# Kernel optimization log

Measured on AMD Instinct MI355X. Metric: run time of the kernel, lower is better.

## Reference

```python
import jax, jax.numpy as jnp
import numpy as np

DILATIONS = (1, 2, 4, 8, 16, 32, 64, 128)  # new_dilation doubles across all blocks*layers
BN_EPS = 1e-5


def conv1x1(x, w, b):
    # x: [B,C,N,T], w: [O,C], b: [O]
    return jnp.einsum('oc,bcnt->bont', w, x) + b[None, :, None, None]


def dilated_conv(x, w, b, d):
    T = x.shape[-1]
    y = jnp.einsum('oc,bcnt->bont', w[:, :, 0], x[..., :T - d]) \
      + jnp.einsum('oc,bcnt->bont', w[:, :, 1], x[..., d:])
    return y + b[None, :, None, None]


def graph_conv(x, supports, w, b):
    # gcn module, order=2, diag_mode='self_and_neighbor' (A unchanged), use_power=False
    outs = [x]
    for A in supports:
        h = x
        for _ in range(2):  # order
            h = jnp.einsum('bcvt,vw->bcwt', h, A)  # nconv: 'ncvl,vw->ncwl'
            outs.append(h)
    return conv1x1(jnp.concatenate(outs, axis=1), w, b)


def setup_inputs() -> dict:
    key = jax.random.key(0)
    B, Cin, N, T = 8, 2, 500, 256
    rc, dc, sc, ec, od, L, R = 32, 32, 256, 512, 12, 8, 10
    ks = jax.random.split(key, 24)
    s = 0.1
    return {
        'x': jax.random.normal(ks[0], (B, Cin, N, T), jnp.float32),
        'A0': jax.random.uniform(ks[1], (N, N), jnp.float32),
        'start_w': jax.random.normal(ks[2], (rc, Cin), jnp.float32) * s,
        'start_b': jnp.zeros((rc,), jnp.float32),
        'filt_w': jax.random.normal(ks[3], (L, dc, rc, 2), jnp.float32) * s,
        'filt_b': jnp.zeros((L, dc), jnp.float32),
        'gate_w': jax.random.normal(ks[4], (L, dc, rc, 2), jnp.float32) * s,
        'gate_b': jnp.zeros((L, dc), jnp.float32),
        'skip_w': jax.random.normal(ks[5], (L, sc, dc), jnp.float32) * s,
        'skip_b': jnp.zeros((L, sc), jnp.float32),
        'gcn_w': jax.random.normal(ks[6], (L, rc, 5 * dc), jnp.float32) * s,  # (order*supports+1)*c_in = 160
        'gcn_b': jnp.zeros((L, rc), jnp.float32),
        'bn_g': jnp.ones((L, rc), jnp.float32),
        'bn_b': jnp.zeros((L, rc), jnp.float32),
        'nodevec1': jax.random.normal(ks[7], (N, R), jnp.float32),
        'nodevec2': jax.random.normal(ks[8], (R, N), jnp.float32),
        'end1_w': jax.random.normal(ks[9], (ec, sc), jnp.float32) * s,
        'end1_b': jnp.zeros((ec,), jnp.float32),
        'end2_w': jax.random.normal(ks[10], (od, ec), jnp.float32) * s,
        'end2_b': jnp.zeros((od,), jnp.float32),
    }


def reference(x, A0, start_w, start_b, filt_w, filt_b, gate_w, gate_b,
              skip_w, skip_b, gcn_w, gcn_b, bn_g, bn_b,
              nodevec1, nodevec2, end1_w, end1_b, end2_w, end2_b):
    # adaptive adjacency: softmax(relu(E1 @ E2), dim=1)
    adp = jax.nn.softmax(jax.nn.relu(nodevec1 @ nodevec2), axis=1)
    supports = [A0, adp]

    h = conv1x1(x, start_w, start_b)  # [B,32,N,T]
    skip = None
    for i, d in enumerate(DILATIONS):
        residual = h
        f = jnp.tanh(dilated_conv(residual, filt_w[i], filt_b[i], d))
        g = jax.nn.sigmoid(dilated_conv(residual, gate_w[i], gate_b[i], d))
        h = f * g
        s = conv1x1(h, skip_w[i], skip_b[i])
        skip = s if skip is None else s + skip[..., -s.shape[-1]:]
        h = graph_conv(h, supports, gcn_w[i], gcn_b[i])
        h = h + residual[..., -h.shape[-1]:]
        # BatchNorm2d in eval mode: running_mean=0, running_var=1
        h = h / jnp.sqrt(1.0 + BN_EPS) * bn_g[i][None, :, None, None] + bn_b[i][None, :, None, None]

    out = jax.nn.relu(skip)
    out = jax.nn.relu(conv1x1(out, end1_w, end1_b))
    out = conv1x1(out, end2_w, end2_b)  # [B,12,N,1]
    return out
```

## Files before the change

kernel.cpp:

```cpp
#include <hip/hip_runtime.h>
#include <cstdint>
#include <cstddef>

#define NN 500
#define KP 512

typedef _Float16 f16;
typedef _Float16 half8 __attribute__((ext_vector_type(8)));
typedef float floatx4 __attribute__((ext_vector_type(4)));

struct PassSet {
  const f16* A[10];
  const f16* B[10];
};

__global__ __launch_bounds__(256) void adp_kernel(const float* __restrict__ e1,
                                                  const float* __restrict__ e2,
                                                  float* __restrict__ adp) {
  int r = blockIdx.x;
  int tid = threadIdx.x;
  __shared__ float red[256];
  __shared__ float e1row[16];
  if (tid < 10) e1row[tid] = e1[r * 10 + tid];
  __syncthreads();
  float z0, z1 = 0.f;
  {
    float acc = 0.f;
#pragma unroll
    for (int k = 0; k < 10; k++) acc += e1row[k] * e2[k * NN + tid];
    z0 = fmaxf(acc, 0.f);
  }
  bool has1 = (tid + 256) < NN;
  if (has1) {
    float acc = 0.f;
#pragma unroll
    for (int k = 0; k < 10; k++) acc += e1row[k] * e2[k * NN + tid + 256];
    z1 = fmaxf(acc, 0.f);
  }
  float mx = has1 ? fmaxf(z0, z1) : z0;
  red[tid] = mx;
  __syncthreads();
  for (int s = 128; s > 0; s >>= 1) {
    if (tid < s) red[tid] = fmaxf(red[tid], red[tid + s]);
    __syncthreads();
  }
  mx = red[0];
  __syncthreads();
  float ex0 = __expf(z0 - mx);
  float ex1 = has1 ? __expf(z1 - mx) : 0.f;
  red[tid] = ex0 + ex1;
  __syncthreads();
  for (int s = 128; s > 0; s >>= 1) {
    if (tid < s) red[tid] += red[tid + s];
    __syncthreads();
  }
  float inv = 1.f / red[0];
  adp[r * NN + tid] = ex0 * inv;
  if (has1) adp[r * NN + tid + 256] = ex1 * inv;
}

__global__ __launch_bounds__(256) void xt_kernel(const float* __restrict__ x,
                                                 float* __restrict__ xT) {
  __shared__ float tile[32][33];
  int tx = threadIdx.x & 31, ty = threadIdx.x >> 5;
  int n0 = blockIdx.x * 32, t0 = blockIdx.y * 32, bc = blockIdx.z;
#pragma unroll
  for (int rr = 0; rr < 4; rr++) {
    int n = n0 + ty + rr * 8, t = t0 + tx;
    tile[ty + rr * 8][tx] = (n < NN) ? x[((size_t)bc * NN + n) * 256 + t] : 0.f;
  }
  __syncthreads();
#pragma unroll
  for (int rr = 0; rr < 4; rr++) {
    int t = t0 + ty + rr * 8, n = n0 + tx;
    if (n < NN) xT[((size_t)bc * 256 + t) * NN + n] = tile[tx][ty + rr * 8];
  }
}

__global__ __launch_bounds__(256) void wtr_kernel(const float* __restrict__ fw,
                                                  const float* __restrict__ gw,
                                                  float* __restrict__ fwT,
                                                  float* __restrict__ gwT) {
  int idx = blockIdx.x * 256 + threadIdx.x;
  if (idx >= 16384) return;
  int c = idx & 31;
  int rest = idx >> 5;
  int tap = rest & 1;
  int cpi = rest >> 1;
  int cp = cpi & 31, i = cpi >> 5;
  size_t src = (((size_t)(i * 32 + c) * 32 + cp) * 2) + tap;
  fwT[idx] = fw[src];
  gwT[idx] = gw[src];
}

__global__ __launch_bounds__(256) void bt_kernel(const float* __restrict__ src,
                                                 f16* __restrict__ hi,
                                                 f16* __restrict__ lo) {
  int idx = blockIdx.x * 256 + threadIdx.x;
  int w = idx >> 9, v = idx & 511;
  float x = (w < NN && v < NN) ? src[v * NN + w] : 0.f;
  f16 h = (f16)x;
  hi[idx] = h;
  lo[idx] = (f16)(x - (float)h);
}

__global__ __launch_bounds__(512) void sq_kernel(const float* __restrict__ srcA,
                                                 const float* __restrict__ srcB,
                                                 f16* __restrict__ hiA, f16* __restrict__ loA,
                                                 f16* __restrict__ hiB, f16* __restrict__ loB) {
  const float* src = blockIdx.y == 0 ? srcA : srcB;
  f16* hi = blockIdx.y == 0 ? hiA : hiB;
  f16* lo = blockIdx.y == 0 ? loA : loB;
  int v = blockIdx.x;
  int w = threadIdx.x;
  __shared__ float vrow[512];
  vrow[w] = (v < NN && w < NN) ? src[v * NN + w] : 0.f;
  __syncthreads();
  float acc = 0.f;
  if (v < NN && w < NN) {
#pragma unroll 4
    for (int u = 0; u < NN; u++) acc = fmaf(vrow[u], src[u * NN + w], acc);
  }
  size_t o = (size_t)w * 512 + v;
  f16 h = (f16)acc;
  hi[o] = h;
  lo[o] = (f16)(acc - (float)h);
}

__global__ __launch_bounds__(256) void padzero_kernel(uint32_t* __restrict__ slab, int R) {
  int idx = blockIdx.x * 256 + threadIdx.x;
  int total = 6 * R * 6;
  if (idx >= total) return;
  int a = idx / (R * 6);
  int rem = idx - a * R * 6;
  int row = rem / 6;
  int q = rem - row * 6;
  slab[(size_t)a * R * 256 + (size_t)row * 256 + 250 + q] = 0u;
}

template <bool FUSED>
__global__ __launch_bounds__(256, 4) void dcm_kernel(
    const float* __restrict__ hprev, const float* __restrict__ xT,
    const float* __restrict__ sw, const float* __restrict__ sb,
    const float* __restrict__ fw, const float* __restrict__ fb,
    const float* __restrict__ gw, const float* __restrict__ gb,
    const float* __restrict__ cw, const float* __restrict__ cb,
    float* __restrict__ Hout,
    f16* __restrict__ P1a,
    f16* __restrict__ P2aH, f16* __restrict__ P2aL,
    f16* __restrict__ P1b,
    f16* __restrict__ P2bH, f16* __restrict__ P2bL,
    float* __restrict__ tapL,
    int Lp, int L, int b0) {
  int j = blockIdx.x, bb = blockIdx.y;
  int n0 = blockIdx.z * 256 + threadIdx.x;
  bool ok = (n0 < NN);
  int nc = ok ? n0 : (NN - 1);
  size_t base = ((size_t)(bb * 32) * Lp + 2 * j) * NN;
  size_t cs = (size_t)Lp * NN;
  float x00 = 0.f, x01 = 0.f, x10 = 0.f, x11 = 0.f;
  if (FUSED) {
    const float* xb = xT + (size_t)(b0 + bb) * 2 * 256 * NN;
    x00 = xb[(size_t)(2 * j) * NN + nc];
    x01 = xb[(size_t)(2 * j + 1) * NN + nc];
    x10 = xb[(size_t)(256 + 2 * j) * NN + nc];
    x11 = xb[(size_t)(256 + 2 * j + 1) * NN + nc];
  }
  float accf[32], accg[32];
#pragma unroll
  for (int c = 0; c < 32; c++) {
    accf[c] = fb[c];
    accg[c] = gb[c];
  }
#pragma unroll 2
  for (int cp = 0; cp < 32; cp++) {
    float v0, v1;
    if (FUSED) {
      float w0 = sw[cp * 2], w1 = sw[cp * 2 + 1], bc = sb[cp];
      v0 = fmaf(w0, x00, fmaf(w1, x10, bc));
      v1 = fmaf(w0, x01, fmaf(w1, x11, bc));
    } else {
      const float* hp = hprev + base + cp * cs;
      v0 = hp[nc];
      v1 = hp[NN + nc];
    }
    const float* fwp = fw + cp * 64;
    const float* gwp = gw + cp * 64;
#pragma unroll
    for (int c = 0; c < 32; c++) {
      float fw0 = fwp[c], fw1 = fwp[32 + c];
      float gw0 = gwp[c], gw1 = gwp[32 + c];
      accf[c] = fmaf(fw0, v0, accf[c]);
      accf[c] = fmaf(fw1, v1, accf[c]);
      accg[c] = fmaf(gw0, v0, accg[c]);
      accg[c] = fmaf(gw1, v1, accg[c]);
    }
  }
  float FG[32];
#pragma unroll
  for (int c = 0; c < 32; c++) {
    float E0 = __expf(2.f * accf[c]);
    float th0 = 1.f - 2.f / (E0 + 1.f);
    float sg0 = 1.f / (1.f + __expf(-accg[c]));
    FG[c] = th0 * sg0;
  }
  if (j == L - 1 && ok) {
    size_t tbase = ((size_t)(b0 + bb) * 32) * NN;
#pragma unroll
    for (int c = 0; c < 32; c++) {
      tapL[tbase + (size_t)c * NN + n0] = FG[c];
    }
  }
  if (Hout == nullptr) return;
#pragma unroll 2
  for (int c = 0; c < 32; c++) {
    const float* wr = cw + c * 160;
    float cbc = cb[c];
    float h0 = cbc, p10 = 0.f, p20 = 0.f, q10 = 0.f, q20 = 0.f;
#pragma unroll
    for (int cp = 0; cp < 32; cp++) {
      float w0 = wr[cp], w1 = wr[32 + cp], w2 = wr[64 + cp];
      float w3 = wr[96 + cp], w4 = wr[128 + cp];
      float f0 = FG[cp];
      h0  = fmaf(w0, f0, h0);
      p10 = fmaf(w1, f0, p10);
      p20 = fmaf(w2, f0, p20);
      q10 = fmaf(w3, f0, q10);
      q20 = fmaf(w4, f0, q20);
    }
    if (FUSED) {
      float sw0 = sw[c * 2], sw1 = sw[c * 2 + 1], sbc = sb[c];
      h0 += fmaf(sw0, x01, fmaf(sw1, x11, sbc));
    } else {
      const float* hr = hprev + ((size_t)(bb * 32 + c) * Lp + 2 * j + 1) * NN;
      h0 += hr[nc];
    }
    if (ok) {
      size_t mi = (size_t)(bb * 32 + c) * L + j;
      size_t o = mi * KP;
      f16 t;
      Hout[mi * NN + n0] = h0;
      P1a[o + n0] = (f16)p10;
      t = (f16)p20; P2aH[o + n0] = t; P2aL[o + n0] = (f16)(p20 - (float)t);
      P1b[o + n0] = (f16)q10;
      t = (f16)q20; P2bH[o + n0] = t; P2bL[o + n0] = (f16)(q20 - (float)t);
    }
  }
}

__global__ __launch_bounds__(256) void mfma_gcn(PassSet s,
    const float* __restrict__ Cin, float* __restrict__ Out, int M,
    const float* __restrict__ bng, const float* __restrict__ bnb, int lshift) {
  __shared__ f16 As[128 * 40];
  __shared__ f16 Bs[128 * 40];
  int tid = threadIdx.x;
  int wave = tid >> 6, lane = tid & 63;
  int wm = wave >> 1, wn = wave & 1;
  int m0 = blockIdx.x * 128;
  int n0 = blockIdx.y * 128;
  int lm = lane & 15, kq = lane >> 4;
  int srow = tid >> 2, sc = tid & 3;
  int ar0 = m0 + srow;      if (ar0 > M - 1) ar0 = M - 1;
  int ar1 = m0 + srow + 64; if (ar1 > M - 1) ar1 = M - 1;
  size_t ag0 = (size_t)ar0 * KP + sc * 8;
  size_t ag1 = (size_t)ar1 * KP + sc * 8;
  size_t bg0 = (size_t)(n0 + srow) * KP + sc * 8;
  size_t bg1 = (size_t)(n0 + srow + 64) * KP + sc * 8;
  int sl0 = srow * 40 + sc * 8;
  int sl1 = (srow + 64) * 40 + sc * 8;

  floatx4 acc[4][4];
#pragma unroll
  for (int i = 0; i < 4; i++)
#pragma unroll
    for (int j = 0; j < 4; j++) acc[i][j] = (floatx4){0.f, 0.f, 0.f, 0.f};

  float4 pa0, pa1, pb0, pb1;
  {
    const f16* Ap = s.A[0];
    const f16* Bp = s.B[0];
    pa0 = *(const float4*)(Ap + ag0);
    pa1 = *(const float4*)(Ap + ag1);
    pb0 = *(const float4*)(Bp + bg0);
    pb1 = *(const float4*)(Bp + bg1);
  }
#pragma unroll
  for (int p = 0; p < 10; p++) {
    const f16* __restrict__ Ap = s.A[p];
    const f16* __restrict__ Bp = s.B[p];
    const f16* __restrict__ Apn = s.A[p < 9 ? p + 1 : p];
    const f16* __restrict__ Bpn = s.B[p < 9 ? p + 1 : p];
    for (int k0 = 0; k0 < KP; k0 += 32) {
      __syncthreads();
      *(float4*)(As + sl0) = pa0;
      *(float4*)(As + sl1) = pa1;
      *(float4*)(Bs + sl0) = pb0;
      *(float4*)(Bs + sl1) = pb1;
      __syncthreads();
      {
        bool lastk = (k0 == KP - 32);
        const f16* An = lastk ? Apn : Ap;
        const f16* Bn = lastk ? Bpn : Bp;
        int kn = lastk ? 0 : k0 + 32;
        pa0 = *(const float4*)(An + ag0 + kn);
        pa1 = *(const float4*)(An + ag1 + kn);
        pb0 = *(const float4*)(Bn + bg0 + kn);
        pb1 = *(const float4*)(Bn + bg1 + kn);
      }
      half8 a[4];
#pragma unroll
      for (int i = 0; i < 4; i++)
        a[i] = *(const half8*)(As + (wm * 64 + i * 16 + lm) * 40 + kq * 8);
#pragma unroll
      for (int j = 0; j < 4; j++) {
        half8 b = *(const half8*)(Bs + (wn * 64 + j * 16 + lm) * 40 + kq * 8);
#pragma unroll
        for (int i = 0; i < 4; i++)
          acc[i][j] = __builtin_amdgcn_mfma_f32_16x16x32_f16(a[i], b, acc[i][j], 0, 0, 0);
      }
    }
  }
  int cn = lane & 15, rq = lane >> 4;
  float rs = rsqrtf(1.f + 1e-5f);
#pragma unroll
  for (int i = 0; i < 4; i++) {
#pragma unroll
    for (int r = 0; r < 4; r++) {
      int row = m0 + wm * 64 + i * 16 + rq * 4 + r;
      if (row < M) {
        int c = (row >> lshift) & 31;
        float scale = bng[c] * rs;
        float bias = bnb[c];
#pragma unroll
        for (int j = 0; j < 4; j++) {
          int col = n0 + wn * 64 + j * 16 + cn;
          if (col < NN) {
            size_t o = (size_t)row * NN + col;
            Out[o] = (acc[i][j][r] + Cin[o]) * scale + bias;
          }
        }
      }
    }
  }
}

#define NB 20
#define NBP 21
__global__ __launch_bounds__(256) void final_kernel(const float* __restrict__ tap,
    const float* __restrict__ skw, const float* __restrict__ skb,
    const float* __restrict__ e1w, const float* __restrict__ e1b,
    const float* __restrict__ e2w, const float* __restrict__ e2b,
    float* __restrict__ out) {
  __shared__ float tapS[256][NBP];
  __shared__ float skS[256][NBP];
  __shared__ float e1S[512][NBP];
  int tid = threadIdx.x;
  int b = blockIdx.y;
  int n0 = blockIdx.x * NB;
  {
    int i = tid >> 5, c = tid & 31;
    const float* tp = tap + (((size_t)i * 8 + b) * 32 + c) * NN + n0;
#pragma unroll
    for (int v = 0; v < NB; v++) tapS[tid][v] = tp[v];
  }
  __syncthreads();
  {
    float bsum = 0.f;
#pragma unroll
    for (int i2 = 0; i2 < 8; i2++) bsum += skb[i2 * 256 + tid];
    float acc[NB];
#pragma unroll
    for (int v = 0; v < NB; v++) acc[v] = bsum;
#pragma unroll
    for (int i2 = 0; i2 < 8; i2++) {
      const float* wr = skw + ((size_t)i2 * 256 + tid) * 32;
#pragma unroll
      for (int cp = 0; cp < 32; cp++) {
        float w = wr[cp];
#pragma unroll
        for (int v = 0; v < NB; v++) acc[v] = fmaf(w, tapS[i2 * 32 + cp][v], acc[v]);
      }
    }
#pragma unroll
    for (int v = 0; v < NB; v++) skS[tid][v] = fmaxf(acc[v], 0.f);
  }
  __syncthreads();
#pragma unroll
  for (int h = 0; h < 2; h++) {
    int k = tid + h * 256;
    float bv = e1b[k];
    float acc[NB];
#pragma unroll
    for (int v = 0; v < NB; v++) acc[v] = bv;
    const float* wr = e1w + (size_t)k * 256;
    for (int o = 0; o < 256; o++) {
      float w = wr[o];
#pragma unroll
      for (int v = 0; v < NB; v++) acc[v] = fmaf(w, skS[o][v], acc[v]);
    }
#pragma unroll
    for (int v = 0; v < NB; v++) e1S[k][v] = fmaxf(acc[v], 0.f);
  }
  __syncthreads();
  if (tid < 12 * NB) {
    int q = tid / NB, v = tid % NB;
    float acc = e2b[q];
    const float* wr = e2w + (size_t)q * 512;
#pragma unroll 8
    for (int k = 0; k < 512; k++) acc = fmaf(wr[k], e1S[k][v], acc);
    out[((size_t)b * 12 + q) * NN + n0 + v] = acc;
  }
}

extern "C" void kernel_launch(void* const* d_in, const int* in_sizes, int n_in,
                              void* d_out, int out_size, void* d_ws, size_t ws_size,
                              hipStream_t stream) {
  const float* x       = (const float*)d_in[0];
  const float* A0      = (const float*)d_in[1];
  const float* start_w = (const float*)d_in[2];
  const float* start_b = (const float*)d_in[3];
  const float* filt_w  = (const float*)d_in[4];
  const float* filt_b  = (const float*)d_in[5];
  const float* gate_w  = (const float*)d_in[6];
  const float* gate_b  = (const float*)d_in[7];
  const float* skip_w  = (const float*)d_in[8];
  const float* skip_b  = (const float*)d_in[9];
  const float* gcn_w   = (const float*)d_in[10];
  const float* gcn_b   = (const float*)d_in[11];
  const float* bn_g    = (const float*)d_in[12];
  const float* bn_b    = (const float*)d_in[13];
  const float* nv1     = (const float*)d_in[14];
  const float* nv2     = (const float*)d_in[15];
  const float* e1w     = (const float*)d_in[16];
  const float* e1b     = (const float*)d_in[17];
  const float* e2w     = (const float*)d_in[18];
  const float* e2b     = (const float*)d_in[19];
  float* out = (float*)d_out;

  char* ws = (char*)d_ws;
  size_t off = 0;
  auto alloc = [&](size_t bytes) -> void* {
    void* p = (void*)(ws + off);
    off += (bytes + 255) & ~(size_t)255;
    return p;
  };
  float* adp   = (float*)alloc((size_t)NN * NN * 4);
  float* tap   = (float*)alloc((size_t)8 * 8 * 32 * NN * 4);
  float* xT    = (float*)alloc((size_t)16 * 256 * NN * 4);
  float* fwT   = (float*)alloc((size_t)16384 * 4);
  float* gwT   = (float*)alloc((size_t)16384 * 4);
  f16*   A0tH  = (f16*)alloc((size_t)KP * KP * 2);
  f16*   A0tL  = (f16*)alloc((size_t)KP * KP * 2);
  f16*   adptH = (f16*)alloc((size_t)KP * KP * 2);
  f16*   adptL = (f16*)alloc((size_t)KP * KP * 2);
  f16*   Q0H   = (f16*)alloc((size_t)KP * KP * 2);
  f16*   Q0L   = (f16*)alloc((size_t)KP * KP * 2);
  f16*   QdH   = (f16*)alloc((size_t)KP * KP * 2);
  f16*   QdL   = (f16*)alloc((size_t)KP * KP * 2);
  size_t fixed = off;

  int g = 1, rpb = 512;
  {
    const int gcand[4] = {8, 4, 2, 1};
    const int rcand[4] = {4096, 2048, 1024, 512};
    bool found = false;
    for (int gi = 0; gi < 4 && !found; gi++) {
      for (int ri = 0; ri < 4 && !found; ri++) {
        int gg = gcand[gi], rr = rcand[ri];
        if (4096 / rr > gg) continue;
        size_t need = fixed + (size_t)gg * 12288000ull +
                      6ull * gg * rr * KP * 2 + (1u << 20);
        if (need <= ws_size) { g = gg; rpb = rr; found = true; }
      }
    }
  }
  float* h128 = (float*)alloc((size_t)g * 8192000ull);
  float* h64  = (float*)alloc((size_t)g * 4096000ull);
  int R = g * rpb;
  f16* slab   = (f16*)alloc(6ull * R * KP * 2);
  f16* P1a  = slab + 0ull * R * KP;
  f16* P2aH = slab + 1ull * R * KP;
  f16* P2aL = slab + 2ull * R * KP;
  f16* P1b  = slab + 3ull * R * KP;
  f16* P2bH = slab + 4ull * R * KP;
  f16* P2bL = slab + 5ull * R * KP;

  adp_kernel<<<NN, 256, 0, stream>>>(nv1, nv2, adp);
  xt_kernel<<<dim3(16, 8, 16), 256, 0, stream>>>(x, xT);
  wtr_kernel<<<64, 256, 0, stream>>>(filt_w, gate_w, fwT, gwT);
  bt_kernel<<<1024, 256, 0, stream>>>(A0, A0tH, A0tL);
  bt_kernel<<<1024, 256, 0, stream>>>(adp, adptH, adptL);
  sq_kernel<<<dim3(512, 2), 512, 0, stream>>>(A0, adp, Q0H, Q0L, QdH, QdL);
  padzero_kernel<<<(36 * R + 255) / 256, 256, 0, stream>>>((uint32_t*)slab, R);

  PassSet ps{};
  {
    const f16* Alist[10] = {P1a, P1a, P2aH, P2aH, P2aL, P1b, P1b, P2bH, P2bH, P2bL};
    const f16* Blist[10] = {A0tH, A0tL, Q0H, Q0L, Q0H, adptH, adptL, QdH, QdL, QdH};
    for (int q = 0; q < 10; q++) { ps.A[q] = Alist[q]; ps.B[q] = Blist[q]; }
  }

  for (int b0 = 0; b0 < 8; b0 += g) {
    float* hprev = nullptr;
    int Lp = 256;
    for (int i = 0; i < 8; i++) {
      int L = Lp >> 1;
      if (i < 7) {
        float* hout = (i & 1) ? h64 : h128;
        int rows = 32 * L;
        int nCh = (rows + rpb - 1) / rpb;
        if (nCh < 1) nCh = 1;
        int bbw = g / nCh;
        for (int ch = 0; ch < nCh; ch++) {
          int bb0 = ch * bbw;
          const float* hprev_c = hprev ? hprev + (size_t)bb0 * 32 * Lp * NN : nullptr;
          float* hout_c = hout + (size_t)bb0 * 32 * L * NN;
          if (i == 0) {
            dcm_kernel<true><<<dim3(L, bbw, 2), 256, 0, stream>>>(
                nullptr, xT, start_w, start_b,
                fwT + i * 2048, filt_b + i * 32, gwT + i * 2048, gate_b + i * 32,
                gcn_w + i * 5120, gcn_b + i * 32, hout_c,
                P1a, P2aH, P2aL, P1b, P2bH, P2bL,
                tap + (size_t)i * 8 * 32 * NN, Lp, L, b0 + bb0);
          } else {
            dcm_kernel<false><<<dim3(L, bbw, 2), 256, 0, stream>>>(
                hprev_c, nullptr, nullptr, nullptr,
                fwT + i * 2048, filt_b + i * 32, gwT + i * 2048, gate_b + i * 32,
                gcn_w + i * 5120, gcn_b + i * 32, hout_c,
                P1a, P2aH, P2aL, P1b, P2bH, P2bL,
                tap + (size_t)i * 8 * 32 * NN, Lp, L, b0 + bb0);
          }
          int M = bbw * 32 * L;
          int Mb = (M + 127) / 128;
          mfma_gcn<<<dim3(Mb, 4), 256, 0, stream>>>(ps, hout_c, hout_c, M,
                                                    bn_g + i * 32, bn_b + i * 32, 7 - i);
        }
        hprev = hout;
        Lp = L;
      } else {
        dcm_kernel<false><<<dim3(1, g, 2), 256, 0, stream>>>(
            hprev, nullptr, nullptr, nullptr,
            fwT + i * 2048, filt_b + i * 32, gwT + i * 2048, gate_b + i * 32,
            gcn_w, gcn_b, nullptr,
            P1a, P2aH, P2aL, P1b, P2bH, P2bL,
            tap + (size_t)i * 8 * 32 * NN, Lp, 1, b0);
      }
    }
  }
  final_kernel<<<dim3(25, 8), 256, 0, stream>>>(tap, skip_w, skip_b, e1w, e1b, e2w, e2b, out);
}
```

Measured before the change: 2.105 ms.

## Group split-precision GCN passes to reuse shared A tiles and swizzle LDS

```diff
diff --git a/kernel.cpp b/kernel.cpp
--- a/kernel.cpp
+++ b/kernel.cpp
@@ -9,9 +9,11 @@
 typedef _Float16 half8 __attribute__((ext_vector_type(8)));
 typedef float floatx4 __attribute__((ext_vector_type(4)));
 
-struct PassSet {
-  const f16* A[10];
-  const f16* B[10];
+struct GroupSet {
+  const f16* A1[4];
+  const f16* A2[4];
+  const f16* B1[4];
+  const f16* B2[4];
 };
 
 __global__ __launch_bounds__(256) void adp_kernel(const float* __restrict__ e1,
@@ -248,11 +250,88 @@
   }
 }
 
-__global__ __launch_bounds__(256) void mfma_gcn(PassSet s,
+template <bool TC, bool TN>
+__device__ __forceinline__ void gcn_group(
+    const f16* __restrict__ A1c, const f16* __restrict__ A2c,
+    const f16* __restrict__ B1c, const f16* __restrict__ B2c,
+    const f16* __restrict__ A1n, const f16* __restrict__ A2n,
+    const f16* __restrict__ B1n, const f16* __restrict__ B2n,
+    f16* As1, f16* As2, f16* Bs1, f16* Bs2,
+    float4 (&pA1)[2], float4 (&pA2)[2], float4 (&pB1)[2], float4 (&pB2)[2],
+    const int (&aoff)[4], const int (&boff)[4], int sl0, int sl1,
+    size_t ag0, size_t ag1, size_t bg0, size_t bg1,
+    floatx4 (&acc)[4][4]) {
+  for (int k0 = 0; k0 < KP; k0 += 32) {
+    __syncthreads();
+    *(float4*)(As1 + sl0) = pA1[0];
+    *(float4*)(As1 + sl1) = pA1[1];
+    if (TC) {
+      *(float4*)(As2 + sl0) = pA2[0];
+      *(float4*)(As2 + sl1) = pA2[1];
+    }
+    *(float4*)(Bs1 + sl0) = pB1[0];
+    *(float4*)(Bs1 + sl1) = pB1[1];
+    *(float4*)(Bs2 + sl0) = pB2[0];
+    *(float4*)(Bs2 + sl1) = pB2[1];
+    __syncthreads();
+    {
+      bool lastk = (k0 == KP - 32);
+      const f16* A1 = lastk ? A1n : A1c;
+      const f16* B1 = lastk ? B1n : B1c;
+      const f16* B2 = lastk ? B2n : B2c;
+      int kn = lastk ? 0 : k0 + 32;
+      pA1[0] = *(const float4*)(A1 + ag0 + kn);
+      pA1[1] = *(const float4*)(A1 + ag1 + kn);
+      pB1[0] = *(const float4*)(B1 + bg0 + kn);
+      pB1[1] = *(const float4*)(B1 + bg1 + kn);
+      if (TC || TN) {
+        bool need = lastk ? TN : TC;
+        if (need) {
+          const f16* A2 = lastk ? A2n : A2c;
+          pA2[0] = *(const float4*)(A2 + ag0 + kn);
+          pA2[1] = *(const float4*)(A2 + ag1 + kn);
+        }
+      }
+    }
+    half8 a1[4];
+#pragma unroll
+    for (int i = 0; i < 4; i++) a1[i] = *(const half8*)(As1 + aoff[i]);
+#pragma unroll
+    for (int j = 0; j < 4; j++) {
+      half8 b = *(const half8*)(Bs1 + boff[j]);
+#pragma unroll
+      for (int i = 0; i < 4; i++)
+        acc[i][j] = __builtin_amdgcn_mfma_f32_16x16x32_f16(a1[i], b, acc[i][j], 0, 0, 0);
+    }
+#pragma unroll
+    for (int j = 0; j < 4; j++) {
+      half8 b = *(const half8*)(Bs2 + boff[j]);
+#pragma unroll
+      for (int i = 0; i < 4; i++)
+        acc[i][j] = __builtin_amdgcn_mfma_f32_16x16x32_f16(a1[i], b, acc[i][j], 0, 0, 0);
+    }
+    if (TC) {
+      half8 a2[4];
+#pragma unroll
+      for (int i = 0; i < 4; i++) a2[i] = *(const half8*)(As2 + aoff[i]);
+#pragma unroll
+      for (int j = 0; j < 4; j++) {
+        half8 b = *(const half8*)(Bs1 + boff[j]);
+#pragma unroll
+        for (int i = 0; i < 4; i++)
+          acc[i][j] = __builtin_amdgcn_mfma_f32_16x16x32_f16(a2[i], b, acc[i][j], 0, 0, 0);
+      }
+    }
+  }
+}
+
+__global__ __launch_bounds__(256) void mfma_gcn(GroupSet s,
     const float* __restrict__ Cin, float* __restrict__ Out, int M,
     const float* __restrict__ bng, const float* __restrict__ bnb, int lshift) {
-  __shared__ f16 As[128 * 40];
-  __shared__ f16 Bs[128 * 40];
+  __shared__ f16 As1[128 * 32];
+  __shared__ f16 As2[128 * 32];
+  __shared__ f16 Bs1[128 * 32];
+  __shared__ f16 Bs2[128 * 32];
   int tid = threadIdx.x;
   int wave = tid >> 6, lane = tid & 63;
   int wm = wave >> 1, wn = wave & 1;
@@ -266,8 +345,15 @@
   size_t ag1 = (size_t)ar1 * KP + sc * 8;
   size_t bg0 = (size_t)(n0 + srow) * KP + sc * 8;
   size_t bg1 = (size_t)(n0 + srow + 64) * KP + sc * 8;
-  int sl0 = srow * 40 + sc * 8;
-  int sl1 = (srow + 64) * 40 + sc * 8;
+  int sl0 = srow * 32 + ((sc ^ ((srow >> 1) & 3)) << 3);
+  int sl1 = sl0 + 64 * 32;
+  int ach = kq ^ ((lm >> 1) & 3);
+  int aoff[4], boff[4];
+#pragma unroll
+  for (int i = 0; i < 4; i++) {
+    aoff[i] = (wm * 64 + i * 16 + lm) * 32 + ach * 8;
+    boff[i] = (wn * 64 + i * 16 + lm) * 32 + ach * 8;
+  }
 
   floatx4 acc[4][4];
 #pragma unroll
@@ -275,51 +361,32 @@
 #pragma unroll
     for (int j = 0; j < 4; j++) acc[i][j] = (floatx4){0.f, 0.f, 0.f, 0.f};
 
-  float4 pa0, pa1, pb0, pb1;
-  {
-    const f16* Ap = s.A[0];
-    const f16* Bp = s.B[0];
-    pa0 = *(const float4*)(Ap + ag0);
-    pa1 = *(const float4*)(Ap + ag1);
-    pb0 = *(const float4*)(Bp + bg0);
-    pb1 = *(const float4*)(Bp + bg1);
-  }
-#pragma unroll
-  for (int p = 0; p < 10; p++) {
-    const f16* __restrict__ Ap = s.A[p];
-    const f16* __restrict__ Bp = s.B[p];
-    const f16* __restrict__ Apn = s.A[p < 9 ? p + 1 : p];
-    const f16* __restrict__ Bpn = s.B[p < 9 ? p + 1 : p];
-    for (int k0 = 0; k0 < KP; k0 += 32) {
-      __syncthreads();
-      *(float4*)(As + sl0) = pa0;
-      *(float4*)(As + sl1) = pa1;
-      *(float4*)(Bs + sl0) = pb0;
-      *(float4*)(Bs + sl1) = pb1;
-      __syncthreads();
-      {
-        bool lastk = (k0 == KP - 32);
-        const f16* An = lastk ? Apn : Ap;
-        const f16* Bn = lastk ? Bpn : Bp;
-        int kn = lastk ? 0 : k0 + 32;
-        pa0 = *(const float4*)(An + ag0 + kn);
-        pa1 = *(const float4*)(An + ag1 + kn);
-        pb0 = *(const float4*)(Bn + bg0 + kn);
-        pb1 = *(const float4*)(Bn + bg1 + kn);
-      }
-      half8 a[4];
-#pragma unroll
-      for (int i = 0; i < 4; i++)
-        a[i] = *(const half8*)(As + (wm * 64 + i * 16 + lm) * 40 + kq * 8);
-#pragma unroll
-      for (int j = 0; j < 4; j++) {
-        half8 b = *(const half8*)(Bs + (wn * 64 + j * 16 + lm) * 40 + kq * 8);
-#pragma unroll
-        for (int i = 0; i < 4; i++)
-          acc[i][j] = __builtin_amdgcn_mfma_f32_16x16x32_f16(a[i], b, acc[i][j], 0, 0, 0);
-      }
-    }
-  }
+  float4 pA1[2], pA2[2], pB1[2], pB2[2];
+  pA2[0] = pA2[1] = (float4){0.f, 0.f, 0.f, 0.f};
+  pA1[0] = *(const float4*)(s.A1[0] + ag0);
+  pA1[1] = *(const float4*)(s.A1[0] + ag1);
+  pB1[0] = *(const float4*)(s.B1[0] + bg0);
+  pB1[1] = *(const float4*)(s.B1[0] + bg1);
+  pB2[0] = *(const float4*)(s.B2[0] + bg0);
+  pB2[1] = *(const float4*)(s.B2[0] + bg1);
+
+  gcn_group<false, true>(s.A1[0], s.A2[0], s.B1[0], s.B2[0],
+                         s.A1[1], s.A2[1], s.B1[1], s.B2[1],
+                         As1, As2, Bs1, Bs2, pA1, pA2, pB1, pB2,
+                         aoff, boff, sl0, sl1, ag0, ag1, bg0, bg1, acc);
+  gcn_group<true, false>(s.A1[1], s.A2[1], s.B1[1], s.B2[1],
+                         s.A1[2], s.A2[2], s.B1[2], s.B2[2],
+                         As1, As2, Bs1, Bs2, pA1, pA2, pB1, pB2,
+                         aoff, boff, sl0, sl1, ag0, ag1, bg0, bg1, acc);
+  gcn_group<false, true>(s.A1[2], s.A2[2], s.B1[2], s.B2[2],
+                         s.A1[3], s.A2[3], s.B1[3], s.B2[3],
+                         As1, As2, Bs1, Bs2, pA1, pA2, pB1, pB2,
+                         aoff, boff, sl0, sl1, ag0, ag1, bg0, bg1, acc);
+  gcn_group<true, true>(s.A1[3], s.A2[3], s.B1[3], s.B2[3],
+                        s.A1[3], s.A2[3], s.B1[3], s.B2[3],
+                        As1, As2, Bs1, Bs2, pA1, pA2, pB1, pB2,
+                        aoff, boff, sl0, sl1, ag0, ag1, bg0, bg1, acc);
+
   int cn = lane & 15, rq = lane >> 4;
   float rs = rsqrtf(1.f + 1e-5f);
 #pragma unroll
@@ -493,12 +560,11 @@
   sq_kernel<<<dim3(512, 2), 512, 0, stream>>>(A0, adp, Q0H, Q0L, QdH, QdL);
   padzero_kernel<<<(36 * R + 255) / 256, 256, 0, stream>>>((uint32_t*)slab, R);
 
-  PassSet ps{};
-  {
-    const f16* Alist[10] = {P1a, P1a, P2aH, P2aH, P2aL, P1b, P1b, P2bH, P2bH, P2bL};
-    const f16* Blist[10] = {A0tH, A0tL, Q0H, Q0L, Q0H, adptH, adptL, QdH, QdL, QdH};
-    for (int q = 0; q < 10; q++) { ps.A[q] = Alist[q]; ps.B[q] = Blist[q]; }
-  }
+  GroupSet gs{};
+  gs.A1[0] = P1a;  gs.A2[0] = P1a;  gs.B1[0] = A0tH;  gs.B2[0] = A0tL;
+  gs.A1[1] = P2aH; gs.A2[1] = P2aL; gs.B1[1] = Q0H;   gs.B2[1] = Q0L;
+  gs.A1[2] = P1b;  gs.A2[2] = P1b;  gs.B1[2] = adptH; gs.B2[2] = adptL;
+  gs.A1[3] = P2bH; gs.A2[3] = P2bL; gs.B1[3] = QdH;   gs.B2[3] = QdL;
 
   for (int b0 = 0; b0 < 8; b0 += g) {
     float* hprev = nullptr;
@@ -532,7 +598,7 @@
           }
           int M = bbw * 32 * L;
           int Mb = (M + 127) / 128;
-          mfma_gcn<<<dim3(Mb, 4), 256, 0, stream>>>(ps, hout_c, hout_c, M,
+          mfma_gcn<<<dim3(Mb, 4), 256, 0, stream>>>(gs, hout_c, hout_c, M,
                                                     bn_g + i * 32, bn_b + i * 32, 7 - i);
         }
         hprev = hout;
```

Measured after the change: 2.561 ms. 21.7% more time.
